# Optimization experiments

Measured on AMD Instinct MI355X. Metric: run time of the kernel, lower is better.

Reference implementation:

```python
import jax, jax.numpy as jnp
import numpy as np
import math

NEG = -1000000.0

def setup_inputs() -> dict:
    key = jax.random.key(0)
    k1, k2, k3, k4 = jax.random.split(key, 4)
    B, S, D = 64, 1024, 64
    query = jax.random.normal(k1, (B, S, D), dtype=jnp.float32)
    key_t = jax.random.normal(k2, (B, S, D), dtype=jnp.float32)
    value = jax.random.normal(k3, (B, S, D), dtype=jnp.float32)
    valid_lens = jax.random.randint(k4, (B,), 1, S + 1, dtype=jnp.int32)
    return {"query": query, "key": key_t, "value": value, "valid_lens": valid_lens}

def reference(query, key, value, valid_lens):
    # query/key/value: [B, S, D]; valid_lens: [B]
    d = query.shape[-1]
    scores = jnp.einsum('bqd,bkd->bqk', query, key) / math.sqrt(d)
    Sk = key.shape[1]
    # 1D valid_lens -> same mask for every query row (repeat_interleave semantics)
    mask = jnp.arange(Sk)[None, None, :] < valid_lens[:, None, None]  # [B,1,Sk]
    scores = jnp.where(mask, scores, NEG)
    weights = jax.nn.softmax(scores, axis=-1)
    # dropout p=0.0 -> identity
    return jnp.einsum('bqk,bkd->bqd', weights, value)
```

## Files before the change

### kernel.cpp

```cpp
#include <hip/hip_runtime.h>
#include <hip/hip_bf16.h>
#include <cstdint>


typedef __attribute__((ext_vector_type(8))) short short8;
typedef __attribute__((ext_vector_type(4))) float f32x4;

#define B_   64
#define S_   1024
#define D_   64
#define BQ   64
#define BK   64
#define KPAD 72

__device__ __forceinline__ uint32_t pk2(float a, float b) {
    float2 t; t.x = a; t.y = b;
    union { __hip_bfloat162 h; uint32_t u; } c;
    c.h = __float22bfloat162_rn(t);
    return c.u;
}

__global__ __launch_bounds__(256, 4)
void attn_fwd(const float* __restrict__ Q, const float* __restrict__ K,
              const float* __restrict__ V, const int* __restrict__ VL,
              float* __restrict__ Out) {
    __shared__ __align__(16) unsigned short lK [BK * KPAD];
    __shared__ __align__(16) unsigned short lVt[D_ * 64];
    __shared__ __align__(16) unsigned short lP [4 * 16 * KPAD];

    const int tid  = threadIdx.x;
    const int wave = tid >> 6;
    const int lane = tid & 63;
    const int col  = lane & 15;
    const int quad = lane >> 4;

    const int bid  = blockIdx.x;
    const int b    = (bid & 7) * 8 + (bid >> 7);
    const int q0   = ((bid >> 3) & 15) * BQ;
    const int vlen = VL[b];
    const int ntiles = (vlen + BK - 1) / BK;

    const int T  = tid >> 4;
    const int m  = tid & 15;
    const int Tl = T & 3;
    const int cb = T >> 2;
    const int dcs = m >> 1;
    const int sws = ((dcs & 1) << 2) | (dcs >> 1);

    const float* Kb = K + (size_t)b * S_ * D_ + 4 * m;
    const float* Vb = V + (size_t)b * S_ * D_ + 4 * m;

    float4 kr[4], vr[4];
    #pragma unroll
    for (int j = 0; j < 4; ++j) {
        const int row = 2 * T + (j >> 1) * 32 + (j & 1);
        kr[j] = *(const float4*)(Kb + (size_t)row * D_);
        vr[j] = *(const float4*)(Vb + (size_t)row * D_);
    }

    short8 qa[2];
    {
        const int qrow = q0 + wave * 16 + col;
        const float* qp = Q + ((size_t)b * S_ + qrow) * D_ + quad * 8;
        #pragma unroll
        for (int c = 0; c < 2; ++c) {
            float4 x0 = *(const float4*)(qp + c * 32);
            float4 x1 = *(const float4*)(qp + c * 32 + 4);
            union { uint32_t u[4]; short8 s; } qq;
            qq.u[0] = pk2(x0.x, x0.y);
            qq.u[1] = pk2(x0.z, x0.w);
            qq.u[2] = pk2(x1.x, x1.y);
            qq.u[3] = pk2(x1.z, x1.w);
            qa[c] = qq.s;
        }
    }

    f32x4 ofrag[4];
    #pragma unroll
    for (int dt = 0; dt < 4; ++dt) ofrag[dt] = (f32x4){0.f, 0.f, 0.f, 0.f};
    float lsum = 0.f;

    const float cexp = 0.18033688011112042f;
    unsigned short* pw = &lP[wave * 16 * KPAD];

    for (int kt = 0; kt < ntiles; ++kt) {
        const int kbase = kt * BK;

        __syncthreads();

        #pragma unroll
        for (int j = 0; j < 4; ++j) {
            const int row = 2 * T + (j >> 1) * 32 + (j & 1);
            uint2 kv;
            kv.x = pk2(kr[j].x, kr[j].y);
            kv.y = pk2(kr[j].z, kr[j].w);
            *(uint2*)&lK[row * KPAD + 4 * m] = kv;
        }
        #pragma unroll
        for (int i = 0; i < 2; ++i) {
            const int p = (cb + 4 * i) ^ sws;
            unsigned short* base = &lVt[p * 8 + 2 * Tl];
            const float4 va = vr[2 * i], vb2 = vr[2 * i + 1];
            *(uint32_t*)&base[(4 * m + 0) * 64] = pk2(va.x, vb2.x);
            *(uint32_t*)&base[(4 * m + 1) * 64] = pk2(va.y, vb2.y);
            *(uint32_t*)&base[(4 * m + 2) * 64] = pk2(va.z, vb2.z);
            *(uint32_t*)&base[(4 * m + 3) * 64] = pk2(va.w, vb2.w);
        }

        __syncthreads();

        if (kt + 1 < ntiles) {
            const size_t off = (size_t)(kt + 1) * BK * D_;
            #pragma unroll
            for (int j = 0; j < 4; ++j) {
                const int row = 2 * T + (j >> 1) * 32 + (j & 1);
                kr[j] = *(const float4*)(Kb + off + (size_t)row * D_);
                vr[j] = *(const float4*)(Vb + off + (size_t)row * D_);
            }
        }

        f32x4 sfrag[4];
        #pragma unroll
        for (int ct = 0; ct < 4; ++ct) {
            f32x4 acc = (f32x4){0.f, 0.f, 0.f, 0.f};
            #pragma unroll
            for (int c = 0; c < 2; ++c) {
                short8 kf = *(const short8*)&lK[(ct * 16 + col) * KPAD + c * 32 + quad * 8];
                acc = __builtin_amdgcn_mfma_f32_16x16x32_bf16(kf, qa[c], acc, 0, 0, 0);
            }
            sfrag[ct] = acc;
        }

        if (kbase + BK <= vlen) {
            #pragma unroll
            for (int ct = 0; ct < 4; ++ct) {
                float e0 = __builtin_amdgcn_exp2f(sfrag[ct][0] * cexp);
                float e1 = __builtin_amdgcn_exp2f(sfrag[ct][1] * cexp);
                float e2 = __builtin_amdgcn_exp2f(sfrag[ct][2] * cexp);
                float e3 = __builtin_amdgcn_exp2f(sfrag[ct][3] * cexp);
                lsum += (e0 + e1) + (e2 + e3);
                uint2 pk; pk.x = pk2(e0, e1); pk.y = pk2(e2, e3);
                *(uint2*)&pw[col * KPAD + ct * 16 + quad * 4] = pk;
            }
        } else {
            #pragma unroll
            for (int ct = 0; ct < 4; ++ct) {
                const int kv0 = kbase + ct * 16 + quad * 4;
                float e[4];
                #pragma unroll
                for (int rr = 0; rr < 4; ++rr) {
                    e[rr] = (kv0 + rr < vlen)
                          ? __builtin_amdgcn_exp2f(sfrag[ct][rr] * cexp) : 0.0f;
                    lsum += e[rr];
                }
                uint2 pk; pk.x = pk2(e[0], e[1]); pk.y = pk2(e[2], e[3]);
                *(uint2*)&pw[col * KPAD + ct * 16 + quad * 4] = pk;
            }
        }

        #pragma unroll
        for (int kc = 0; kc < 2; ++kc) {
            short8 pa = *(const short8*)&pw[col * KPAD + kc * 32 + quad * 8];
            #pragma unroll
            for (int dt = 0; dt < 4; ++dt) {
                const int sr = ((col >> 3) << 2) | dt;
                const int p  = (kc * 4 + quad) ^ sr;
                short8 vb = *(const short8*)&lVt[(dt * 16 + col) * 64 + p * 8];
                ofrag[dt] = __builtin_amdgcn_mfma_f32_16x16x32_bf16(pa, vb, ofrag[dt], 0, 0, 0);
            }
        }
    }

    float s = lsum;
    s += __shfl_xor(s, 16, 64);
    s += __shfl_xor(s, 32, 64);
    const int qrow0 = q0 + wave * 16 + quad * 4;
    #pragma unroll
    for (int rr = 0; rr < 4; ++rr) {
        const float inv = 1.0f / __shfl(s, quad * 4 + rr, 64);
        float* op = Out + ((size_t)b * S_ + qrow0 + rr) * D_ + col;
        #pragma unroll
        for (int dt = 0; dt < 4; ++dt)
            op[dt * 16] = ofrag[dt][rr] * inv;
    }
}

extern "C" void kernel_launch(void* const* d_in, const int* in_sizes, int n_in,
                              void* d_out, int out_size, void* d_ws, size_t ws_size,
                              hipStream_t stream) {
    const float* Q  = (const float*)d_in[0];
    const float* K  = (const float*)d_in[1];
    const float* V  = (const float*)d_in[2];
    const int*   VL = (const int*)d_in[3];
    float* Out = (float*)d_out;
    dim3 grid(B_ * (S_ / BQ));
    attn_fwd<<<grid, 256, 0, stream>>>(Q, K, V, VL, Out);
}
```

Before: 115.4 us.

## Schedule attention work items longest-first via persistent blocks and atomic queue

A small pre-kernel ranks batches by valid length and writes a work list ordered longest-first. The attention kernel becomes persistent, with 768 blocks that pull items from the list through an atomic counter, and its launch bounds drop from 4 to 3 blocks per CU. The aim is to remove the load imbalance caused by variable valid_lens. The cost is an extra kernel launch, atomic traffic, and a different occupancy target.

```diff
diff --git a/kernel.cpp b/kernel.cpp
--- a/kernel.cpp
+++ b/kernel.cpp
@@ -12,6 +12,8 @@
 #define BQ   64
 #define BK   64
 #define KPAD 72
+#define NITEMS (B_ * (S_ / BQ))
+#define NBLOCKS 768
 
 __device__ __forceinline__ uint32_t pk2(float a, float b) {
     float2 t; t.x = a; t.y = b;
@@ -20,25 +22,38 @@
     return c.u;
 }
 
-__global__ __launch_bounds__(256, 4)
+__global__ void sched_k(const int* __restrict__ VL, uint32_t* __restrict__ ws) {
+    const int i = threadIdx.x;
+    __shared__ int vls[B_];
+    vls[i] = VL[i];
+    __syncthreads();
+    const int v = vls[i];
+    int r = 0;
+    #pragma unroll 8
+    for (int j = 0; j < B_; ++j) {
+        const int u = vls[j];
+        r += (u > v) || (u == v && j < i);
+    }
+    #pragma unroll
+    for (int q = 0; q < 16; ++q)
+        ws[16 + r * 16 + q] = (uint32_t)((i << 4) | q);
+    if (i == 0) ws[0] = 0;
+}
+
+__global__ __launch_bounds__(256, 3)
 void attn_fwd(const float* __restrict__ Q, const float* __restrict__ K,
               const float* __restrict__ V, const int* __restrict__ VL,
-              float* __restrict__ Out) {
+              float* __restrict__ Out, uint32_t* __restrict__ ws) {
     __shared__ __align__(16) unsigned short lK [BK * KPAD];
     __shared__ __align__(16) unsigned short lVt[D_ * 64];
     __shared__ __align__(16) unsigned short lP [4 * 16 * KPAD];
+    __shared__ int sIdx;
 
     const int tid  = threadIdx.x;
     const int wave = tid >> 6;
     const int lane = tid & 63;
     const int col  = lane & 15;
     const int quad = lane >> 4;
-
-    const int bid  = blockIdx.x;
-    const int b    = (bid & 7) * 8 + (bid >> 7);
-    const int q0   = ((bid >> 3) & 15) * BQ;
-    const int vlen = VL[b];
-    const int ntiles = (vlen + BK - 1) / BK;
 
     const int T  = tid >> 4;
     const int m  = tid & 15;
@@ -47,141 +62,156 @@
     const int dcs = m >> 1;
     const int sws = ((dcs & 1) << 2) | (dcs >> 1);
 
-    const float* Kb = K + (size_t)b * S_ * D_ + 4 * m;
-    const float* Vb = V + (size_t)b * S_ * D_ + 4 * m;
-
-    float4 kr[4], vr[4];
-    #pragma unroll
-    for (int j = 0; j < 4; ++j) {
-        const int row = 2 * T + (j >> 1) * 32 + (j & 1);
-        kr[j] = *(const float4*)(Kb + (size_t)row * D_);
-        vr[j] = *(const float4*)(Vb + (size_t)row * D_);
-    }
-
-    short8 qa[2];
-    {
-        const int qrow = q0 + wave * 16 + col;
-        const float* qp = Q + ((size_t)b * S_ + qrow) * D_ + quad * 8;
-        #pragma unroll
-        for (int c = 0; c < 2; ++c) {
-            float4 x0 = *(const float4*)(qp + c * 32);
-            float4 x1 = *(const float4*)(qp + c * 32 + 4);
-            union { uint32_t u[4]; short8 s; } qq;
-            qq.u[0] = pk2(x0.x, x0.y);
-            qq.u[1] = pk2(x0.z, x0.w);
-            qq.u[2] = pk2(x1.x, x1.y);
-            qq.u[3] = pk2(x1.z, x1.w);
-            qa[c] = qq.s;
-        }
-    }
-
-    f32x4 ofrag[4];
-    #pragma unroll
-    for (int dt = 0; dt < 4; ++dt) ofrag[dt] = (f32x4){0.f, 0.f, 0.f, 0.f};
-    float lsum = 0.f;
-
     const float cexp = 0.18033688011112042f;
     unsigned short* pw = &lP[wave * 16 * KPAD];
-
-    for (int kt = 0; kt < ntiles; ++kt) {
-        const int kbase = kt * BK;
-
+    const uint32_t* items = ws + 16;
+
+    for (;;) {
         __syncthreads();
-
+        if (tid == 0) sIdx = (int)atomicAdd(&ws[0], 1u);
+        __syncthreads();
+        const int idx = sIdx;
+        if (idx >= NITEMS) break;
+
+        const uint32_t it = items[idx];
+        const int b    = (int)(it >> 4);
+        const int q0   = (int)(it & 15) * BQ;
+        const int vlen = VL[b];
+        const int ntiles = (vlen + BK - 1) / BK;
+
+        const float* Kb = K + (size_t)b * S_ * D_ + 4 * m;
+        const float* Vb = V + (size_t)b * S_ * D_ + 4 * m;
+
+        float4 kr[4], vr[4];
         #pragma unroll
         for (int j = 0; j < 4; ++j) {
             const int row = 2 * T + (j >> 1) * 32 + (j & 1);
-            uint2 kv;
-            kv.x = pk2(kr[j].x, kr[j].y);
-            kv.y = pk2(kr[j].z, kr[j].w);
-            *(uint2*)&lK[row * KPAD + 4 * m] = kv;
-        }
+            kr[j] = *(const float4*)(Kb + (size_t)row * D_);
+            vr[j] = *(const float4*)(Vb + (size_t)row * D_);
+        }
+
+        short8 qa[2];
+        {
+            const int qrow = q0 + wave * 16 + col;
+            const float* qp = Q + ((size_t)b * S_ + qrow) * D_ + quad * 8;
+            #pragma unroll
+            for (int c = 0; c < 2; ++c) {
+                float4 x0 = *(const float4*)(qp + c * 32);
+                float4 x1 = *(const float4*)(qp + c * 32 + 4);
+                union { uint32_t u[4]; short8 s; } qq;
+                qq.u[0] = pk2(x0.x, x0.y);
+                qq.u[1] = pk2(x0.z, x0.w);
+                qq.u[2] = pk2(x1.x, x1.y);
+                qq.u[3] = pk2(x1.z, x1.w);
+                qa[c] = qq.s;
+            }
+        }
+
+        f32x4 ofrag[4];
         #pragma unroll
-        for (int i = 0; i < 2; ++i) {
-            const int p = (cb + 4 * i) ^ sws;
-            unsigned short* base = &lVt[p * 8 + 2 * Tl];
-            const float4 va = vr[2 * i], vb2 = vr[2 * i + 1];
-            *(uint32_t*)&base[(4 * m + 0) * 64] = pk2(va.x, vb2.x);
-            *(uint32_t*)&base[(4 * m + 1) * 64] = pk2(va.y, vb2.y);
-            *(uint32_t*)&base[(4 * m + 2) * 64] = pk2(va.z, vb2.z);
-            *(uint32_t*)&base[(4 * m + 3) * 64] = pk2(va.w, vb2.w);
-        }
-
-        __syncthreads();
-
-        if (kt + 1 < ntiles) {
-            const size_t off = (size_t)(kt + 1) * BK * D_;
+        for (int dt = 0; dt < 4; ++dt) ofrag[dt] = (f32x4){0.f, 0.f, 0.f, 0.f};
+        float lsum = 0.f;
+
+        for (int kt = 0; kt < ntiles; ++kt) {
+            const int kbase = kt * BK;
+
+            __syncthreads();
+
             #pragma unroll
             for (int j = 0; j < 4; ++j) {
                 const int row = 2 * T + (j >> 1) * 32 + (j & 1);
-                kr[j] = *(const float4*)(Kb + off + (size_t)row * D_);
-                vr[j] = *(const float4*)(Vb + off + (size_t)row * D_);
-            }
-        }
-
-        f32x4 sfrag[4];
+                uint2 kv;
+                kv.x = pk2(kr[j].x, kr[j].y);
+                kv.y = pk2(kr[j].z, kr[j].w);
+                *(uint2*)&lK[row * KPAD + 4 * m] = kv;
+            }
+            #pragma unroll
+            for (int i = 0; i < 2; ++i) {
+                const int p = (cb + 4 * i) ^ sws;
+                unsigned short* base = &lVt[p * 8 + 2 * Tl];
+                const float4 va = vr[2 * i], vb2 = vr[2 * i + 1];
+                *(uint32_t*)&base[(4 * m + 0) * 64] = pk2(va.x, vb2.x);
+                *(uint32_t*)&base[(4 * m + 1) * 64] = pk2(va.y, vb2.y);
+                *(uint32_t*)&base[(4 * m + 2) * 64] = pk2(va.z, vb2.z);
+                *(uint32_t*)&base[(4 * m + 3) * 64] = pk2(va.w, vb2.w);
+            }
+
+            __syncthreads();
+
+            if (kt + 1 < ntiles) {
+                const size_t off = (size_t)(kt + 1) * BK * D_;
+                #pragma unroll
+                for (int j = 0; j < 4; ++j) {
+                    const int row = 2 * T + (j >> 1) * 32 + (j & 1);
+                    kr[j] = *(const float4*)(Kb + off + (size_t)row * D_);
+                    vr[j] = *(const float4*)(Vb + off + (size_t)row * D_);
+                }
+            }
+
+            f32x4 sfrag[4];
+            #pragma unroll
+            for (int ct = 0; ct < 4; ++ct) {
+                f32x4 acc = (f32x4){0.f, 0.f, 0.f, 0.f};
+                #pragma unroll
+                for (int c = 0; c < 2; ++c) {
+                    short8 kf = *(const short8*)&lK[(ct * 16 + col) * KPAD + c * 32 + quad * 8];
+                    acc = __builtin_amdgcn_mfma_f32_16x16x32_bf16(kf, qa[c], acc, 0, 0, 0);
+                }
+                sfrag[ct] = acc;
+            }
+
+            if (kbase + BK <= vlen) {
+                #pragma unroll
+                for (int ct = 0; ct < 4; ++ct) {
+                    float e0 = __builtin_amdgcn_exp2f(sfrag[ct][0] * cexp);
+                    float e1 = __builtin_amdgcn_exp2f(sfrag[ct][1] * cexp);
+                    float e2 = __builtin_amdgcn_exp2f(sfrag[ct][2] * cexp);
+                    float e3 = __builtin_amdgcn_exp2f(sfrag[ct][3] * cexp);
+                    lsum += (e0 + e1) + (e2 + e3);
+                    uint2 pk; pk.x = pk2(e0, e1); pk.y = pk2(e2, e3);
+                    *(uint2*)&pw[col * KPAD + ct * 16 + quad * 4] = pk;
+                }
+            } else {
+                #pragma unroll
+                for (int ct = 0; ct < 4; ++ct) {
+                    const int kv0 = kbase + ct * 16 + quad * 4;
+                    float e[4];
+                    #pragma unroll
+                    for (int rr = 0; rr < 4; ++rr) {
+                        e[rr] = (kv0 + rr < vlen)
+                              ? __builtin_amdgcn_exp2f(sfrag[ct][rr] * cexp) : 0.0f;
+                        lsum += e[rr];
+                    }
+                    uint2 pk; pk.x = pk2(e[0], e[1]); pk.y = pk2(e[2], e[3]);
+                    *(uint2*)&pw[col * KPAD + ct * 16 + quad * 4] = pk;
+                }
+            }
+
+            #pragma unroll
+            for (int kc = 0; kc < 2; ++kc) {
+                short8 pa = *(const short8*)&pw[col * KPAD + kc * 32 + quad * 8];
+                #pragma unroll
+                for (int dt = 0; dt < 4; ++dt) {
+                    const int sr = ((col >> 3) << 2) | dt;
+                    const int p  = (kc * 4 + quad) ^ sr;
+                    short8 vb = *(const short8*)&lVt[(dt * 16 + col) * 64 + p * 8];
+                    ofrag[dt] = __builtin_amdgcn_mfma_f32_16x16x32_bf16(pa, vb, ofrag[dt], 0, 0, 0);
+                }
+            }
+        }
+
+        float s = lsum;
+        s += __shfl_xor(s, 16, 64);
+        s += __shfl_xor(s, 32, 64);
+        const int qrow0 = q0 + wave * 16 + quad * 4;
         #pragma unroll
-        for (int ct = 0; ct < 4; ++ct) {
-            f32x4 acc = (f32x4){0.f, 0.f, 0.f, 0.f};
-            #pragma unroll
-            for (int c = 0; c < 2; ++c) {
-                short8 kf = *(const short8*)&lK[(ct * 16 + col) * KPAD + c * 32 + quad * 8];
-                acc = __builtin_amdgcn_mfma_f32_16x16x32_bf16(kf, qa[c], acc, 0, 0, 0);
-            }
-            sfrag[ct] = acc;
-        }
-
-        if (kbase + BK <= vlen) {
-            #pragma unroll
-            for (int ct = 0; ct < 4; ++ct) {
-                float e0 = __builtin_amdgcn_exp2f(sfrag[ct][0] * cexp);
-                float e1 = __builtin_amdgcn_exp2f(sfrag[ct][1] * cexp);
-                float e2 = __builtin_amdgcn_exp2f(sfrag[ct][2] * cexp);
-                float e3 = __builtin_amdgcn_exp2f(sfrag[ct][3] * cexp);
-                lsum += (e0 + e1) + (e2 + e3);
-                uint2 pk; pk.x = pk2(e0, e1); pk.y = pk2(e2, e3);
-                *(uint2*)&pw[col * KPAD + ct * 16 + quad * 4] = pk;
-            }
-        } else {
-            #pragma unroll
-            for (int ct = 0; ct < 4; ++ct) {
-                const int kv0 = kbase + ct * 16 + quad * 4;
-                float e[4];
-                #pragma unroll
-                for (int rr = 0; rr < 4; ++rr) {
-                    e[rr] = (kv0 + rr < vlen)
-                          ? __builtin_amdgcn_exp2f(sfrag[ct][rr] * cexp) : 0.0f;
-                    lsum += e[rr];
-                }
-                uint2 pk; pk.x = pk2(e[0], e[1]); pk.y = pk2(e[2], e[3]);
-                *(uint2*)&pw[col * KPAD + ct * 16 + quad * 4] = pk;
-            }
-        }
-
-        #pragma unroll
-        for (int kc = 0; kc < 2; ++kc) {
-            short8 pa = *(const short8*)&pw[col * KPAD + kc * 32 + quad * 8];
-            #pragma unroll
-            for (int dt = 0; dt < 4; ++dt) {
-                const int sr = ((col >> 3) << 2) | dt;
-                const int p  = (kc * 4 + quad) ^ sr;
-                short8 vb = *(const short8*)&lVt[(dt * 16 + col) * 64 + p * 8];
-                ofrag[dt] = __builtin_amdgcn_mfma_f32_16x16x32_bf16(pa, vb, ofrag[dt], 0, 0, 0);
-            }
-        }
-    }
-
-    float s = lsum;
-    s += __shfl_xor(s, 16, 64);
-    s += __shfl_xor(s, 32, 64);
-    const int qrow0 = q0 + wave * 16 + quad * 4;
-    #pragma unroll
-    for (int rr = 0; rr < 4; ++rr) {
-        const float inv = 1.0f / __shfl(s, quad * 4 + rr, 64);
-        float* op = Out + ((size_t)b * S_ + qrow0 + rr) * D_ + col;
-        #pragma unroll
-        for (int dt = 0; dt < 4; ++dt)
-            op[dt * 16] = ofrag[dt][rr] * inv;
+        for (int rr = 0; rr < 4; ++rr) {
+            const float inv = 1.0f / __shfl(s, quad * 4 + rr, 64);
+            float* op = Out + ((size_t)b * S_ + qrow0 + rr) * D_ + col;
+            #pragma unroll
+            for (int dt = 0; dt < 4; ++dt)
+                op[dt * 16] = ofrag[dt][rr] * inv;
+        }
     }
 }
 
@@ -193,6 +223,8 @@
     const float* V  = (const float*)d_in[2];
     const int*   VL = (const int*)d_in[3];
     float* Out = (float*)d_out;
-    dim3 grid(B_ * (S_ / BQ));
-    attn_fwd<<<grid, 256, 0, stream>>>(Q, K, V, VL, Out);
-}
+    uint32_t* ws = (uint32_t*)d_ws;
+
+    sched_k<<<1, 64, 0, stream>>>(VL, ws);
+    attn_fwd<<<NBLOCKS, 256, 0, stream>>>(Q, K, V, VL, Out, ws);
+}
```

Result: slower. 123.8 us (+7.3%).

## Pre-pack K and V into bf16 MFMA fragment layout in a separate kernel

Applied to the files above, without the earlier changes.

Adds a pre-pass kernel that converts K and V to bf16 once and writes them to the workspace already arranged in per-lane MFMA operand order (V transposed). The attention kernel then loads K/V fragments straight from global memory with short8 loads, with no LDS staging, no per-block fp32-to-bf16 conversion, and no __syncthreads per tile. The aim is to stop each of the 16 query blocks per batch from re-converting K/V and to shrink LDS use. The cost is an extra launch, a workspace round trip, and fragment loads in the inner loop that now have global latency instead of prefetched registers.

```diff
diff --git a/kernel.cpp b/kernel.cpp
--- a/kernel.cpp
+++ b/kernel.cpp
@@ -12,6 +12,7 @@
 #define BQ   64
 #define BK   64
 #define KPAD 72
+#define VP_OFF (4u * 1024u * 1024u)
 
 __device__ __forceinline__ uint32_t pk2(float a, float b) {
     float2 t; t.x = a; t.y = b;
@@ -19,14 +20,58 @@
     c.h = __float22bfloat162_rn(t);
     return c.u;
 }
+__device__ __forceinline__ unsigned short f2bf(float f) {
+    union { float f; uint32_t u; } v; v.f = f;
+    return (unsigned short)((v.u + 0x7fffu + ((v.u >> 16) & 1u)) >> 16);
+}
+
+__global__ __launch_bounds__(256)
+void pack_k(const float* __restrict__ K, const float* __restrict__ V,
+            const int* __restrict__ VL, unsigned short* __restrict__ ws) {
+    const int bid = blockIdx.x;
+    const int b = bid >> 4, kt = bid & 15;
+    if (kt * BK >= VL[b]) return;
+    __shared__ unsigned short sK [BK * 68];
+    __shared__ unsigned short sVt[D_ * 68];
+
+    const int t = threadIdx.x;
+    const int r = t >> 2, cb4 = (t & 3) * 16;
+    const float* kp = K + ((size_t)b * S_ + kt * BK + r) * D_ + cb4;
+    const float* vp = V + ((size_t)b * S_ + kt * BK + r) * D_ + cb4;
+    #pragma unroll
+    for (int j4 = 0; j4 < 4; ++j4) {
+        float4 kx = *(const float4*)(kp + j4 * 4);
+        uint2 kv; kv.x = pk2(kx.x, kx.y); kv.y = pk2(kx.z, kx.w);
+        *(uint2*)&sK[r * 68 + cb4 + j4 * 4] = kv;
+        float4 vx = *(const float4*)(vp + j4 * 4);
+        sVt[(cb4 + j4 * 4 + 0) * 68 + r] = f2bf(vx.x);
+        sVt[(cb4 + j4 * 4 + 1) * 68 + r] = f2bf(vx.y);
+        sVt[(cb4 + j4 * 4 + 2) * 68 + r] = f2bf(vx.z);
+        sVt[(cb4 + j4 * 4 + 3) * 68 + r] = f2bf(vx.w);
+    }
+    __syncthreads();
+
+    const int lane = t & 63, il = t >> 6;
+    const int col = lane & 15, quad = lane >> 4;
+    const size_t tbase = (size_t)bid * 4096 + lane * 8;
+    unsigned short* Kp = ws;
+    unsigned short* Vp = ws + VP_OFF;
+    #pragma unroll
+    for (int i = 0; i < 2; ++i) {
+        const int inst = i * 4 + il;
+        const int ct = inst >> 1, c = inst & 1;
+        short8 kk = *(const short8*)&sK[(ct * 16 + col) * 68 + c * 32 + quad * 8];
+        *(short8*)(Kp + tbase + inst * 512) = kk;
+        const int kc = inst >> 2, dt = inst & 3;
+        short8 vv = *(const short8*)&sVt[(dt * 16 + col) * 68 + kc * 32 + quad * 8];
+        *(short8*)(Vp + tbase + inst * 512) = vv;
+    }
+}
 
 __global__ __launch_bounds__(256, 4)
-void attn_fwd(const float* __restrict__ Q, const float* __restrict__ K,
-              const float* __restrict__ V, const int* __restrict__ VL,
-              float* __restrict__ Out) {
-    __shared__ __align__(16) unsigned short lK [BK * KPAD];
-    __shared__ __align__(16) unsigned short lVt[D_ * 64];
-    __shared__ __align__(16) unsigned short lP [4 * 16 * KPAD];
+void attn_fwd(const float* __restrict__ Q, const int* __restrict__ VL,
+              float* __restrict__ Out, const unsigned short* __restrict__ ws) {
+    __shared__ __align__(16) unsigned short lP[4 * 16 * KPAD];
 
     const int tid  = threadIdx.x;
     const int wave = tid >> 6;
@@ -40,23 +85,8 @@
     const int vlen = VL[b];
     const int ntiles = (vlen + BK - 1) / BK;
 
-    const int T  = tid >> 4;
-    const int m  = tid & 15;
-    const int Tl = T & 3;
-    const int cb = T >> 2;
-    const int dcs = m >> 1;
-    const int sws = ((dcs & 1) << 2) | (dcs >> 1);
-
-    const float* Kb = K + (size_t)b * S_ * D_ + 4 * m;
-    const float* Vb = V + (size_t)b * S_ * D_ + 4 * m;
-
-    float4 kr[4], vr[4];
-    #pragma unroll
-    for (int j = 0; j < 4; ++j) {
-        const int row = 2 * T + (j >> 1) * 32 + (j & 1);
-        kr[j] = *(const float4*)(Kb + (size_t)row * D_);
-        vr[j] = *(const float4*)(Vb + (size_t)row * D_);
-    }
+    const unsigned short* Kp = ws + (size_t)b * 16 * 4096 + lane * 8;
+    const unsigned short* Vp = Kp + VP_OFF;
 
     short8 qa[2];
     {
@@ -84,53 +114,21 @@
     unsigned short* pw = &lP[wave * 16 * KPAD];
 
     for (int kt = 0; kt < ntiles; ++kt) {
-        const int kbase = kt * BK;
-
-        __syncthreads();
-
-        #pragma unroll
-        for (int j = 0; j < 4; ++j) {
-            const int row = 2 * T + (j >> 1) * 32 + (j & 1);
-            uint2 kv;
-            kv.x = pk2(kr[j].x, kr[j].y);
-            kv.y = pk2(kr[j].z, kr[j].w);
-            *(uint2*)&lK[row * KPAD + 4 * m] = kv;
-        }
-        #pragma unroll
-        for (int i = 0; i < 2; ++i) {
-            const int p = (cb + 4 * i) ^ sws;
-            unsigned short* base = &lVt[p * 8 + 2 * Tl];
-            const float4 va = vr[2 * i], vb2 = vr[2 * i + 1];
-            *(uint32_t*)&base[(4 * m + 0) * 64] = pk2(va.x, vb2.x);
-            *(uint32_t*)&base[(4 * m + 1) * 64] = pk2(va.y, vb2.y);
-            *(uint32_t*)&base[(4 * m + 2) * 64] = pk2(va.z, vb2.z);
-            *(uint32_t*)&base[(4 * m + 3) * 64] = pk2(va.w, vb2.w);
-        }
-
-        __syncthreads();
-
-        if (kt + 1 < ntiles) {
-            const size_t off = (size_t)(kt + 1) * BK * D_;
-            #pragma unroll
-            for (int j = 0; j < 4; ++j) {
-                const int row = 2 * T + (j >> 1) * 32 + (j & 1);
-                kr[j] = *(const float4*)(Kb + off + (size_t)row * D_);
-                vr[j] = *(const float4*)(Vb + off + (size_t)row * D_);
-            }
-        }
+        const unsigned short* kq = Kp + (size_t)kt * 4096;
+        const unsigned short* vq = Vp + (size_t)kt * 4096;
 
         f32x4 sfrag[4];
         #pragma unroll
         for (int ct = 0; ct < 4; ++ct) {
+            short8 k0 = *(const short8*)(kq + (ct * 2 + 0) * 512);
+            short8 k1 = *(const short8*)(kq + (ct * 2 + 1) * 512);
             f32x4 acc = (f32x4){0.f, 0.f, 0.f, 0.f};
-            #pragma unroll
-            for (int c = 0; c < 2; ++c) {
-                short8 kf = *(const short8*)&lK[(ct * 16 + col) * KPAD + c * 32 + quad * 8];
-                acc = __builtin_amdgcn_mfma_f32_16x16x32_bf16(kf, qa[c], acc, 0, 0, 0);
-            }
+            acc = __builtin_amdgcn_mfma_f32_16x16x32_bf16(k0, qa[0], acc, 0, 0, 0);
+            acc = __builtin_amdgcn_mfma_f32_16x16x32_bf16(k1, qa[1], acc, 0, 0, 0);
             sfrag[ct] = acc;
         }
 
+        const int kbase = kt * BK;
         if (kbase + BK <= vlen) {
             #pragma unroll
             for (int ct = 0; ct < 4; ++ct) {
@@ -163,9 +161,7 @@
             short8 pa = *(const short8*)&pw[col * KPAD + kc * 32 + quad * 8];
             #pragma unroll
             for (int dt = 0; dt < 4; ++dt) {
-                const int sr = ((col >> 3) << 2) | dt;
-                const int p  = (kc * 4 + quad) ^ sr;
-                short8 vb = *(const short8*)&lVt[(dt * 16 + col) * 64 + p * 8];
+                short8 vb = *(const short8*)(vq + (kc * 4 + dt) * 512);
                 ofrag[dt] = __builtin_amdgcn_mfma_f32_16x16x32_bf16(pa, vb, ofrag[dt], 0, 0, 0);
             }
         }
@@ -193,6 +189,8 @@
     const float* V  = (const float*)d_in[2];
     const int*   VL = (const int*)d_in[3];
     float* Out = (float*)d_out;
-    dim3 grid(B_ * (S_ / BQ));
-    attn_fwd<<<grid, 256, 0, stream>>>(Q, K, V, VL, Out);
+    unsigned short* ws = (unsigned short*)d_ws;
+
+    pack_k  <<<B_ * 16, 256, 0, stream>>>(K, V, VL, ws);
+    attn_fwd<<<B_ * 16, 256, 0, stream>>>(Q, VL, Out, ws);
 }
```

After: 123.5 us. 7.0% more time.
